# Kernel optimization log

Hardware: AMD Instinct MI355X
Metric: run time of the kernel (lower is better)

## Reference

```python
import jax, jax.numpy as jnp
import numpy as np

NUM_HEADS = 8
LN_EPS = 1e-5


def layer_norm_chw(x, w, b):
    # LayerNorm over (C, H, W) jointly, elementwise affine of shape (C, H, W)
    mu = jnp.mean(x, axis=(1, 2, 3), keepdims=True)
    var = jnp.mean(jnp.square(x - mu), axis=(1, 2, 3), keepdims=True)
    return (x - mu) * jax.lax.rsqrt(var + LN_EPS) * w[None] + b[None]


def conv1x1(x, w, b):
    # 1x1 conv == per-pixel matmul. x: (B,C,H,W), w: (O,C), b: (O,)
    return jnp.einsum('bcxy,oc->boxy', x, w) + b[None, :, None, None]


def setup_inputs() -> dict:
    key = jax.random.key(0)
    ks = jax.random.split(key, 8)
    B, C, H, W = 16, 512, 64, 64
    Dq, Dv, Dh = 512, 512, 2048
    s = lambda fan_in: 1.0 / np.sqrt(fan_in)
    return {
        'x': jax.random.normal(ks[0], (B, C, H, W), jnp.float32),
        'ln1_w': jnp.ones((C, H, W), jnp.float32),
        'ln1_b': jnp.zeros((C, H, W), jnp.float32),
        'q_w': jax.random.normal(ks[1], (Dq, C), jnp.float32) * s(C),
        'q_b': jnp.zeros((Dq,), jnp.float32),
        'k_w': jax.random.normal(ks[2], (Dq, C), jnp.float32) * s(C),
        'k_b': jnp.zeros((Dq,), jnp.float32),
        'v_w': jax.random.normal(ks[3], (Dv, C), jnp.float32) * s(C),
        'v_b': jnp.zeros((Dv,), jnp.float32),
        'hu_w': jax.random.normal(ks[4], (C, Dv), jnp.float32) * s(Dv),
        'hu_b': jnp.zeros((C,), jnp.float32),
        'ln2_w': jnp.ones((C, H, W), jnp.float32),
        'ln2_b': jnp.zeros((C, H, W), jnp.float32),
        'ff1_w': jax.random.normal(ks[5], (Dh, C), jnp.float32) * s(C),
        'ff1_b': jnp.zeros((Dh,), jnp.float32),
        'ff2_w': jax.random.normal(ks[6], (C, Dh), jnp.float32) * s(Dh),
        'ff2_b': jnp.zeros((C,), jnp.float32),
    }


def reference(x, ln1_w, ln1_b, q_w, q_b, k_w, k_b, v_w, v_b,
              hu_w, hu_b, ln2_w, ln2_b, ff1_w, ff1_b, ff2_w, ff2_b):
    B, C, H, W = x.shape
    h = NUM_HEADS

    a = layer_norm_chw(x, ln1_w, ln1_b)
    Q = conv1x1(a, q_w, q_b)   # (B, Dq, H, W)
    K = conv1x1(a, k_w, k_b)   # (B, Dq, H, W)
    V = conv1x1(a, v_w, v_b)   # (B, Dv, H, W)

    Dq, Dv = Q.shape[1], V.shape[1]
    # softmax over channel dim for Q (per pixel, over all Dq channels)
    Q = jax.nn.softmax(Q, axis=1)
    # softmax over flattened spatial dim for K (per channel)
    K = jax.nn.softmax(K.reshape(B, Dq, H * W), axis=-1).reshape(B, Dq, H, W)

    # split heads: (B, h, d, H, W)
    Qh = Q.reshape(B, h, Dq // h, H, W)
    Kh = K.reshape(B, h, Dq // h, H, W)
    Vh = V.reshape(B, h, Dv // h, H, W)

    # linear attention: KV = sum_xy K ⊗ V, then per-pixel KV^T @ Q
    KV = jnp.einsum('bhkxy,bhvxy->bhkv', Kh, Vh)        # (B, h, dq, dv)
    attn = jnp.einsum('bhkv,bhkxy->bhvxy', KV, Qh)      # (B, h, dv, H, W)
    attn = attn.reshape(B, Dv, H, W)
    attn = conv1x1(attn, hu_w, hu_b)                    # (B, C, H, W)

    x = x + attn
    x = layer_norm_chw(x, ln2_w, ln2_b)
    ff = conv1x1(jax.nn.gelu(conv1x1(x, ff1_w, ff1_b), approximate=False), ff2_w, ff2_b)
    return x + ff
```

## Files before the change

kernel.cpp:

```cpp
#include <hip/hip_runtime.h>
#include <math.h>

#define BATCH 16
#define CCH   512
#define HWS   4096
#define CHW   (CCH*HWS)
#define DHFF  2048
#define NHEAD 8
#define HD    64
#define QKVLD 1536
#define LNEPS 1e-5f

typedef unsigned short u16;
typedef __bf16 bf16x8 __attribute__((ext_vector_type(8)));
typedef float f32x4 __attribute__((ext_vector_type(4)));

__device__ __forceinline__ float gelu_f(float x) {
    float y = 1.5957691216057308f * x * (1.0f + 0.044715f * x * x);
    return x / (1.0f + __expf(-y));
}
__device__ __forceinline__ u16 f2bf(float f) {
    union { float f; unsigned u; } c; c.f = f;
    unsigned r = c.u + 0x7FFFu + ((c.u >> 16) & 1u);
    return (u16)(r >> 16);
}
__device__ __forceinline__ float bf2f(u16 h) {
    union { unsigned u; float f; } c; c.u = ((unsigned)h) << 16; return c.f;
}
__device__ __forceinline__ void gld16(const u16* g, u16* l) {
    __builtin_amdgcn_global_load_lds((const __attribute__((address_space(1))) unsigned*)g,
                                     (__attribute__((address_space(3))) unsigned*)l, 16, 0, 0);
}

__global__ __launch_bounds__(256) void stats_k(const float* __restrict__ src,
                                               float* __restrict__ st) {
    int b = blockIdx.y;
    const float4* p = (const float4*)(src + (size_t)b * CHW + (size_t)blockIdx.x * (CHW / 64));
    float s = 0.f, ss = 0.f;
    for (int i = threadIdx.x; i < (CHW / 64 / 4); i += 256) {
        float4 v = p[i];
        s  += v.x + v.y + v.z + v.w;
        ss += v.x * v.x + v.y * v.y + v.z * v.z + v.w * v.w;
    }
    __shared__ float r1[256], r2[256];
    int t = threadIdx.x;
    r1[t] = s; r2[t] = ss; __syncthreads();
    for (int o = 128; o > 0; o >>= 1) {
        if (t < o) { r1[t] += r1[t + o]; r2[t] += r2[t + o]; }
        __syncthreads();
    }
    if (t == 0) { atomicAdd(&st[2 * b], r1[0]); atomicAdd(&st[2 * b + 1], r2[0]); }
}

__global__ __launch_bounds__(256) void cvt_k(const float* __restrict__ src,
                                             u16* __restrict__ dst, int n4) {
    int i = blockIdx.x * 256 + threadIdx.x;
    if (i >= n4) return;
    float4 v = ((const float4*)src)[i];
    uint2 o; u16* op = (u16*)&o;
    op[0] = f2bf(v.x); op[1] = f2bf(v.y); op[2] = f2bf(v.z); op[3] = f2bf(v.w);
    ((uint2*)dst)[i] = o;
}

__global__ __launch_bounds__(256) void tr_k(const float* __restrict__ src,
                                            float* __restrict__ dst) {
    int p0 = blockIdx.x * 32, c0 = blockIdx.y * 32;
    __shared__ float T[32][33];
    int tx = threadIdx.x & 31, ty = threadIdx.x >> 5;
#pragma unroll
    for (int i = 0; i < 4; ++i)
        T[ty + i * 8][tx] = src[(size_t)(c0 + ty + i * 8) * HWS + p0 + tx];
    __syncthreads();
#pragma unroll
    for (int i = 0; i < 4; ++i)
        dst[(size_t)(p0 + ty + i * 8) * CCH + c0 + tx] = T[tx][ty + i * 8];
}

__global__ __launch_bounds__(256) void ln1t_k(const float* __restrict__ x,
                                              const float* __restrict__ w,
                                              const float* __restrict__ bb,
                                              const float* __restrict__ st,
                                              u16* __restrict__ a, int cb) {
    int p0 = blockIdx.x * 32, c0 = blockIdx.y * 32, bl = blockIdx.z;
    int b = cb + bl;
    float mean = st[2 * b] * (1.0f / CHW);
    float var  = st[2 * b + 1] * (1.0f / CHW) - mean * mean;
    float rstd = rsqrtf(var + LNEPS);
    __shared__ float T[32][33];
    int tx = threadIdx.x & 31, ty = threadIdx.x >> 5;
    const float* xb = x + (size_t)b * CHW;
#pragma unroll
    for (int i = 0; i < 4; ++i) {
        size_t o = (size_t)(c0 + ty + i * 8) * HWS + p0 + tx;
        T[ty + i * 8][tx] = (xb[o] - mean) * rstd * w[o] + bb[o];
    }
    __syncthreads();
    u16* ab = a + (size_t)bl * CHW;
#pragma unroll
    for (int i = 0; i < 4; ++i)
        ab[(size_t)(p0 + ty + i * 8) * CCH + c0 + tx] = f2bf(T[tx][ty + i * 8]);
}

template<int ACT, int OBF>
__global__ __launch_bounds__(256) void gemm_tn(const u16* __restrict__ A,
                                               const u16* __restrict__ B,
                                               const float* __restrict__ bias,
                                               void* __restrict__ Out,
                                               int K, int ldo, int nt) {
    __shared__ u16 As[128 * 32];
    __shared__ u16 Bs[128 * 32];
    const int tid = threadIdx.x;
    const int cpx = gridDim.x >> 3;
    const int wg = (blockIdx.x & 7) * cpx + (blockIdx.x >> 3);
    const int m0 = (wg / nt) * 128;
    const int n0 = (wg % nt) * 128;
    const int lane = tid & 63;
    const int w = tid >> 6;
    const int wm = (w & 1) * 64, wn = (w >> 1) * 64;
    const int ls = lane & 15, lq = lane >> 4;

    f32x4 acc[4][4];
#pragma unroll
    for (int i = 0; i < 4; ++i)
#pragma unroll
        for (int j = 0; j < 4; ++j) acc[i][j] = (f32x4){0.f, 0.f, 0.f, 0.f};

    const int srow = w * 16 + (lane >> 2);
    const int scol = (lane & 3) * 8;
    const u16* gA0 = A + (size_t)(m0 + srow) * K + scol;
    const u16* gA1 = gA0 + (size_t)64 * K;
    const u16* gB0 = B + (size_t)(n0 + srow) * K + scol;
    const u16* gB1 = gB0 + (size_t)64 * K;
    u16* lA0 = As + w * 512;
    u16* lA1 = As + 2048 + w * 512;
    u16* lB0 = Bs + w * 512;
    u16* lB1 = Bs + 2048 + w * 512;

    for (int kt = 0; kt < K; kt += 32) {
        __syncthreads();
        gld16(gA0 + kt, lA0);
        gld16(gA1 + kt, lA1);
        gld16(gB0 + kt, lB0);
        gld16(gB1 + kt, lB1);
        __syncthreads();
        bf16x8 af[4], bfv[4];
#pragma unroll
        for (int i = 0; i < 4; ++i)
            af[i] = *(bf16x8*)&As[(wm + i * 16 + ls) * 32 + lq * 8];
#pragma unroll
        for (int j = 0; j < 4; ++j)
            bfv[j] = *(bf16x8*)&Bs[(wn + j * 16 + ls) * 32 + lq * 8];
#pragma unroll
        for (int i = 0; i < 4; ++i)
#pragma unroll
            for (int j = 0; j < 4; ++j)
                acc[i][j] = __builtin_amdgcn_mfma_f32_16x16x32_bf16(bfv[j], af[i], acc[i][j], 0, 0, 0);
    }

#pragma unroll
    for (int j = 0; j < 4; ++j) {
        int nb = n0 + wn + j * 16 + lq * 4;
        float4 bv = *(const float4*)&bias[nb];
#pragma unroll
        for (int i = 0; i < 4; ++i) {
            int m = m0 + wm + i * 16 + ls;
            float v0 = acc[i][j][0] + bv.x;
            float v1 = acc[i][j][1] + bv.y;
            float v2 = acc[i][j][2] + bv.z;
            float v3 = acc[i][j][3] + bv.w;
            if (ACT) { v0 = gelu_f(v0); v1 = gelu_f(v1); v2 = gelu_f(v2); v3 = gelu_f(v3); }
            size_t idx = (size_t)m * ldo + nb;
            if (OBF) {
                uint2 o; u16* op = (u16*)&o;
                op[0] = f2bf(v0); op[1] = f2bf(v1); op[2] = f2bf(v2); op[3] = f2bf(v3);
                *(uint2*)((u16*)Out + idx) = o;
            } else {
                *(float4*)((float*)Out + idx) = (float4){v0, v1, v2, v3};
            }
        }
    }
}

__global__ __launch_bounds__(256) void softmax_row_k(u16* __restrict__ QKV) {
    int m = blockIdx.x * 4 + (threadIdx.x >> 6);
    int lane = threadIdx.x & 63;
    u16* row = QKV + (size_t)m * QKVLD + lane * 8;
    uint4 raw = *(uint4*)row;
    u16* pr = (u16*)&raw;
    float v[8];
#pragma unroll
    for (int i = 0; i < 8; ++i) v[i] = bf2f(pr[i]);
    float mx = v[0];
#pragma unroll
    for (int i = 1; i < 8; ++i) mx = fmaxf(mx, v[i]);
    for (int o = 32; o > 0; o >>= 1) mx = fmaxf(mx, __shfl_xor(mx, o, 64));
    float s = 0.f;
#pragma unroll
    for (int i = 0; i < 8; ++i) { v[i] = __expf(v[i] - mx); s += v[i]; }
    for (int o = 32; o > 0; o >>= 1) s += __shfl_xor(s, o, 64);
    float inv = 1.0f / s;
#pragma unroll
    for (int i = 0; i < 8; ++i) pr[i] = f2bf(v[i] * inv);
    *(uint4*)row = raw;
}

__global__ __launch_bounds__(256) void kcolstat_k(const u16* __restrict__ QKV,
                                                  float* __restrict__ kpart) {
    int pc = blockIdx.x, bl = blockIdx.y;
    int cg = threadIdx.x & 63;
    int ps = threadIdx.x >> 6;
    const u16* base = QKV + (size_t)bl * HWS * QKVLD + CCH + cg * 8;
    int p0 = pc * 256 + ps * 64;
    float m[8];
#pragma unroll
    for (int i = 0; i < 8; ++i) m[i] = -1e30f;
    for (int p = p0; p < p0 + 64; ++p) {
        uint4 r = *(const uint4*)(base + (size_t)p * QKVLD);
        u16* rp = (u16*)&r;
#pragma unroll
        for (int i = 0; i < 8; ++i) m[i] = fmaxf(m[i], bf2f(rp[i]));
    }
    __shared__ float red[4][512];
#pragma unroll
    for (int i = 0; i < 8; ++i) red[ps][cg * 8 + i] = m[i];
    __syncthreads();
#pragma unroll
    for (int i = 0; i < 8; ++i)
        m[i] = fmaxf(fmaxf(red[0][cg * 8 + i], red[1][cg * 8 + i]),
                     fmaxf(red[2][cg * 8 + i], red[3][cg * 8 + i]));
    __syncthreads();
    float s[8];
#pragma unroll
    for (int i = 0; i < 8; ++i) s[i] = 0.f;
    for (int p = p0; p < p0 + 64; ++p) {
        uint4 r = *(const uint4*)(base + (size_t)p * QKVLD);
        u16* rp = (u16*)&r;
#pragma unroll
        for (int i = 0; i < 8; ++i) s[i] += __expf(bf2f(rp[i]) - m[i]);
    }
#pragma unroll
    for (int i = 0; i < 8; ++i) red[ps][cg * 8 + i] = s[i];
    __syncthreads();
    if (ps == 0) {
        float* outp = kpart + (((size_t)bl * 16 + pc) * 512 + cg * 8) * 2;
#pragma unroll
        for (int i = 0; i < 8; ++i) {
            float sv = red[0][cg * 8 + i] + red[1][cg * 8 + i] +
                       red[2][cg * 8 + i] + red[3][cg * 8 + i];
            outp[2 * i] = m[i]; outp[2 * i + 1] = sv;
        }
    }
}

__global__ __launch_bounds__(256) void kcolmerge_k(const float* __restrict__ kpart,
                                                   float* __restrict__ kstat) {
    int bl = blockIdx.x;
#pragma unroll
    for (int j = 0; j < 2; ++j) {
        int col = threadIdx.x * 2 + j;
        float m = -1e30f;
        for (int pc = 0; pc < 16; ++pc)
            m = fmaxf(m, kpart[(((size_t)bl * 16 + pc) * 512 + col) * 2]);
        float s = 0.f;
        for (int pc = 0; pc < 16; ++pc) {
            const float* p = kpart + (((size_t)bl * 16 + pc) * 512 + col) * 2;
            s += p[1] * __expf(p[0] - m);
        }
        kstat[((size_t)bl * 512 + col) * 2]     = m;
        kstat[((size_t)bl * 512 + col) * 2 + 1] = 1.0f / s;
    }
}

__global__ __launch_bounds__(256) void kv_k2(const u16* __restrict__ QKV,
                                             const float* __restrict__ kstat,
                                             float* __restrict__ KV) {
    int pc = blockIdx.x, h = blockIdx.y, bl = blockIdx.z;
    const u16* kbase = QKV + (size_t)bl * HWS * QKVLD + CCH + h * HD;
    const u16* vbase = kbase + CCH;
    float* kvb = KV + ((size_t)bl * NHEAD + h) * (HD * HD);
    __shared__ float Ks[64][65], Vs[64][65];
    __shared__ float Ms[64], Is[64];
    int tid = threadIdx.x;
    if (tid < 64) {
        const float* sp = kstat + ((size_t)bl * 512 + h * HD + tid) * 2;
        Ms[tid] = sp[0]; Is[tid] = sp[1];
    }
    int tk = tid >> 4, tv = tid & 15;
    float acc[4][4];
#pragma unroll
    for (int i = 0; i < 4; ++i)
#pragma unroll
        for (int j = 0; j < 4; ++j) acc[i][j] = 0.f;

    for (int s = 0; s < 4; ++s) {
        int pbase = pc * 256 + s * 64;
        __syncthreads();
#pragma unroll
        for (int j = 0; j < 2; ++j) {
            int li = tid + j * 256;
            int pl = li >> 3, c8 = (li & 7) * 8;
            uint4 kr = *(const uint4*)(kbase + (size_t)(pbase + pl) * QKVLD + c8);
            uint4 vr = *(const uint4*)(vbase + (size_t)(pbase + pl) * QKVLD + c8);
            u16* kp = (u16*)&kr; u16* vp = (u16*)&vr;
#pragma unroll
            for (int t = 0; t < 8; ++t) {
                Ks[pl][c8 + t] = __expf(bf2f(kp[t]) - Ms[c8 + t]) * Is[c8 + t];
                Vs[pl][c8 + t] = bf2f(vp[t]);
            }
        }
        __syncthreads();
#pragma unroll 4
        for (int p = 0; p < 64; ++p) {
            float ka[4], va[4];
#pragma unroll
            for (int i = 0; i < 4; ++i) { ka[i] = Ks[p][tk * 4 + i]; va[i] = Vs[p][tv * 4 + i]; }
#pragma unroll
            for (int i = 0; i < 4; ++i)
#pragma unroll
                for (int j = 0; j < 4; ++j) acc[i][j] += ka[i] * va[j];
        }
    }
#pragma unroll
    for (int i = 0; i < 4; ++i)
#pragma unroll
        for (int j = 0; j < 4; ++j)
            atomicAdd(&kvb[(size_t)(tk * 4 + i) * HD + tv * 4 + j], acc[i][j]);
}

__global__ __launch_bounds__(256) void attn_k2(const u16* __restrict__ QKV,
                                               const float* __restrict__ KV,
                                               u16* __restrict__ attnRaw) {
    int pt = blockIdx.x, h = blockIdx.y, bl = blockIdx.z;
    const u16* qbase = QKV + (size_t)bl * HWS * QKVLD + h * HD;
    const float* kvb = KV + ((size_t)bl * NHEAD + h) * (HD * HD);
    __shared__ float KVs[64][68], Qs[64][68];
    int tid = threadIdx.x;
#pragma unroll
    for (int j = 0; j < 4; ++j) {
        int li = tid + j * 256;
        int k = li >> 4, c4 = (li & 15) * 4;
        *(float4*)&KVs[k][c4] = *(const float4*)(kvb + (size_t)k * HD + c4);
    }
#pragma unroll
    for (int j = 0; j < 2; ++j) {
        int li = tid + j * 256;
        int pl = li >> 3, c8 = (li & 7) * 8;
        uint4 qr = *(const uint4*)(qbase + (size_t)(pt * 64 + pl) * QKVLD + c8);
        u16* qp = (u16*)&qr;
#pragma unroll
        for (int t = 0; t < 8; ++t) Qs[pl][c8 + t] = bf2f(qp[t]);
    }
    __syncthreads();
    int tp = tid >> 4, tv = tid & 15;
    float acc[4][4];
#pragma unroll
    for (int i = 0; i < 4; ++i)
#pragma unroll
        for (int j = 0; j < 4; ++j) acc[i][j] = 0.f;
#pragma unroll 4
    for (int k = 0; k < 64; ++k) {
        float qa[4], kv4[4];
#pragma unroll
        for (int i = 0; i < 4; ++i) { qa[i] = Qs[tp * 4 + i][k]; kv4[i] = KVs[k][tv * 4 + i]; }
#pragma unroll
        for (int i = 0; i < 4; ++i)
#pragma unroll
            for (int j = 0; j < 4; ++j) acc[i][j] += qa[i] * kv4[j];
    }
#pragma unroll
    for (int i = 0; i < 4; ++i) {
        uint2 wv; u16* wp = (u16*)&wv;
#pragma unroll
        for (int j = 0; j < 4; ++j) wp[j] = f2bf(acc[i][j]);
        *(uint2*)(attnRaw + (size_t)(bl * HWS + pt * 64 + tp * 4 + i) * CCH + h * HD + tv * 4) = wv;
    }
}

__global__ __launch_bounds__(256) void resid_t_k(const float* __restrict__ x,
                                                 const float* __restrict__ ao,
                                                 float* __restrict__ r,
                                                 float* __restrict__ pstat, int cb) {
    int p0 = blockIdx.x * 32, c0 = blockIdx.y * 32, bl = blockIdx.z;
    int b = cb + bl;
    __shared__ float T[32][33];
    __shared__ float r1[256], r2[256];
    int tx = threadIdx.x & 31, ty = threadIdx.x >> 5;
    const float* xb = x + (size_t)b * CHW;
#pragma unroll
    for (int i = 0; i < 4; ++i)
        T[ty + i * 8][tx] = xb[(size_t)(c0 + ty + i * 8) * HWS + p0 + tx];
    __syncthreads();
    float s = 0.f, ss = 0.f;
#pragma unroll
    for (int i = 0; i < 4; ++i) {
        size_t o = (size_t)bl * CHW + (size_t)(p0 + ty + i * 8) * CCH + c0 + tx;
        float v = T[tx][ty + i * 8] + ao[o];
        r[o] = v; s += v; ss += v * v;
    }
    int t = threadIdx.x;
    r1[t] = s; r2[t] = ss; __syncthreads();
    for (int o = 128; o > 0; o >>= 1) {
        if (t < o) { r1[t] += r1[t + o]; r2[t] += r2[t + o]; }
        __syncthreads();
    }
    if (t == 0) {
        float* pp = pstat + ((size_t)b * 2048 + (size_t)blockIdx.x * 16 + blockIdx.y) * 2;
        pp[0] = r1[0]; pp[1] = r2[0];
    }
}

__global__ __launch_bounds__(256) void red2_k(const float* __restrict__ pstat,
                                              float* __restrict__ st, int cb) {
    int b = cb + blockIdx.x;
    const float* p = pstat + (size_t)b * 4096;
    float s = 0.f, ss = 0.f;
    for (int i = threadIdx.x; i < 2048; i += 256) {
        s += p[2 * i]; ss += p[2 * i + 1];
    }
    __shared__ float r1[256], r2[256];
    int t = threadIdx.x;
    r1[t] = s; r2[t] = ss; __syncthreads();
    for (int o = 128; o > 0; o >>= 1) {
        if (t < o) { r1[t] += r1[t + o]; r2[t] += r2[t + o]; }
        __syncthreads();
    }
    if (t == 0) { st[32 + 2 * b] = r1[0]; st[32 + 2 * b + 1] = r2[0]; }
}

__global__ __launch_bounds__(256) void ln2a_k(const float* __restrict__ r,
                                              const float* __restrict__ w2t,
                                              const float* __restrict__ b2t,
                                              const float* __restrict__ st,
                                              u16* __restrict__ x2, int cb) {
    size_t i4 = (size_t)blockIdx.x * 256 + threadIdx.x;
    int bl = (int)(i4 / (CHW / 4));
    int b = cb + bl;
    size_t off4 = i4 % (CHW / 4);
    float mean = st[32 + 2 * b] * (1.0f / CHW);
    float var  = st[32 + 2 * b + 1] * (1.0f / CHW) - mean * mean;
    float rstd = rsqrtf(var + LNEPS);
    float4 v  = ((const float4*)(r + (size_t)bl * CHW))[off4];
    float4 wv = ((const float4*)w2t)[off4];
    float4 bv = ((const float4*)b2t)[off4];
    uint2 o; u16* op = (u16*)&o;
    op[0] = f2bf((v.x - mean) * rstd * wv.x + bv.x);
    op[1] = f2bf((v.y - mean) * rstd * wv.y + bv.y);
    op[2] = f2bf((v.z - mean) * rstd * wv.z + bv.z);
    op[3] = f2bf((v.w - mean) * rstd * wv.w + bv.w);
    ((uint2*)(x2 + (size_t)bl * CHW))[off4] = o;
}

__global__ __launch_bounds__(256) void final_t_k(const u16* __restrict__ x2,
                                                 const float* __restrict__ ffo,
                                                 float* __restrict__ out, int cb) {
    int c0 = blockIdx.x * 32, p0 = blockIdx.y * 32, bl = blockIdx.z;
    int b = cb + bl;
    __shared__ float T[32][33];
    int tx = threadIdx.x & 31, ty = threadIdx.x >> 5;
#pragma unroll
    for (int i = 0; i < 4; ++i) {
        size_t o = (size_t)bl * CHW + (size_t)(p0 + ty + i * 8) * CCH + c0 + tx;
        T[ty + i * 8][tx] = ffo[o] + bf2f(x2[o]);
    }
    __syncthreads();
    float* ob = out + (size_t)b * CHW;
#pragma unroll
    for (int i = 0; i < 4; ++i)
        ob[(size_t)(c0 + ty + i * 8) * HWS + p0 + tx] = T[tx][ty + i * 8];
}

extern "C" void kernel_launch(void* const* d_in, const int* in_sizes, int n_in,
                              void* d_out, int out_size, void* d_ws, size_t ws_size,
                              hipStream_t stream) {
    const float* x    = (const float*)d_in[0];
    const float* ln1w = (const float*)d_in[1];
    const float* ln1b = (const float*)d_in[2];
    const float* qw   = (const float*)d_in[3];
    const float* qb   = (const float*)d_in[4];
    const float* kw   = (const float*)d_in[5];
    const float* kb   = (const float*)d_in[6];
    const float* vw   = (const float*)d_in[7];
    const float* vb   = (const float*)d_in[8];
    const float* huw  = (const float*)d_in[9];
    const float* hub  = (const float*)d_in[10];
    const float* ln2w = (const float*)d_in[11];
    const float* ln2b = (const float*)d_in[12];
    const float* f1w  = (const float*)d_in[13];
    const float* f1b  = (const float*)d_in[14];
    const float* f2w  = (const float*)d_in[15];
    const float* f2b  = (const float*)d_in[16];
    float* out = (float*)d_out;
    float* ws = (float*)d_ws;

    float* stats = ws;
    float* qkvb  = ws + 64;
    u16*   wqkv  = (u16*)(ws + 1600);
    u16*   whu   = (u16*)(ws + 394816);
    u16*   wf1   = (u16*)(ws + 525888);
    u16*   wf2   = (u16*)(ws + 1050176);
    float* w2t   = ws + 1574464;
    float* b2t   = ws + 3671616;
    float* pstat = ws + 5768768;
    float* kpart = ws + 5834304;
    float* kstat = ws + 6096448;
    float* kvbuf = ws + 6112832;

    int G = 16;
    while (G > 1 && (6112832ull + (size_t)G * 7372800ull) * 4ull > ws_size) G >>= 1;
    const int nch = BATCH / G;
    const size_t U = (size_t)G * CHW;

    float* R       = kvbuf + (size_t)G * 32768;
    u16*   a_bf    = (u16*)R;
    u16*   QKVb    = (u16*)(R + U / 2);
    float* attnOut = R + U / 2;
    float* rbuf    = R + 3 * U / 2;
    u16*   x2bf    = (u16*)R;
    u16*   Hbuf    = (u16*)(R + U / 2);
    float* ffOut   = R + 5 * U / 2;

    hipMemsetAsync(stats, 0, 64 * sizeof(float), stream);

    cvt_k<<<dim3(256), 256, 0, stream>>>(qw, wqkv, 65536);
    cvt_k<<<dim3(256), 256, 0, stream>>>(kw, wqkv + 262144, 65536);
    cvt_k<<<dim3(256), 256, 0, stream>>>(vw, wqkv + 524288, 65536);
    cvt_k<<<dim3(256), 256, 0, stream>>>(huw, whu, 65536);
    cvt_k<<<dim3(1024), 256, 0, stream>>>(f1w, wf1, 262144);
    cvt_k<<<dim3(1024), 256, 0, stream>>>(f2w, wf2, 262144);
    tr_k<<<dim3(128, 16), 256, 0, stream>>>(ln2w, w2t);
    tr_k<<<dim3(128, 16), 256, 0, stream>>>(ln2b, b2t);
    hipMemcpyAsync(qkvb,        qb, 512 * sizeof(float), hipMemcpyDeviceToDevice, stream);
    hipMemcpyAsync(qkvb + 512,  kb, 512 * sizeof(float), hipMemcpyDeviceToDevice, stream);
    hipMemcpyAsync(qkvb + 1024, vb, 512 * sizeof(float), hipMemcpyDeviceToDevice, stream);

    stats_k<<<dim3(64, BATCH), 256, 0, stream>>>(x, stats);

    for (int g = 0; g < nch; ++g) {
        const int cb = g * G;
        const int mt = G * 32;
        ln1t_k<<<dim3(128, 16, G), 256, 0, stream>>>(x, ln1w, ln1b, stats, a_bf, cb);
        gemm_tn<0, 1><<<dim3(mt * 12), 256, 0, stream>>>(a_bf, wqkv, qkvb, QKVb, CCH, QKVLD, 12);
        softmax_row_k<<<dim3(G * 1024), 256, 0, stream>>>(QKVb);
        kcolstat_k<<<dim3(16, G), 256, 0, stream>>>(QKVb, kpart);
        kcolmerge_k<<<dim3(G), 256, 0, stream>>>(kpart, kstat);
        hipMemsetAsync(kvbuf, 0, (size_t)G * 32768 * sizeof(float), stream);
        kv_k2<<<dim3(16, NHEAD, G), 256, 0, stream>>>(QKVb, kstat, kvbuf);
        attn_k2<<<dim3(64, NHEAD, G), 256, 0, stream>>>(QKVb, kvbuf, a_bf);
        gemm_tn<0, 0><<<dim3(mt * 4), 256, 0, stream>>>(a_bf, whu, hub, attnOut, CCH, CCH, 4);
        resid_t_k<<<dim3(128, 16, G), 256, 0, stream>>>(x, attnOut, rbuf, pstat, cb);
        red2_k<<<dim3(G), 256, 0, stream>>>(pstat, stats, cb);
        ln2a_k<<<dim3(G * 2048), 256, 0, stream>>>(rbuf, w2t, b2t, stats, x2bf, cb);
        gemm_tn<1, 1><<<dim3(mt * 16), 256, 0, stream>>>(x2bf, wf1, f1b, Hbuf, CCH, DHFF, 16);
        gemm_tn<0, 0><<<dim3(mt * 4), 256, 0, stream>>>(Hbuf, wf2, f2b, ffOut, DHFF, CCH, 4);
        final_t_k<<<dim3(16, 128, G), 256, 0, stream>>>(x2bf, ffOut, out, cb);
    }
}
```

Before: 1.571 ms.

## Double-buffer LDS tiles in GEMM to overlap global loads with MFMA

Gives the bf16 GEMM kernel two LDS buffers for the A and B tiles. The next K-slice is prefetched with direct-to-LDS loads while MFMAs run on the current slice, and the per-iteration barrier count drops from two to one. The aim is to hide global memory latency behind compute, at the cost of doubling LDS use per block, which may lower occupancy.

```diff
diff --git a/kernel.cpp b/kernel.cpp
--- a/kernel.cpp
+++ b/kernel.cpp
@@ -107,8 +107,8 @@
                                                const float* __restrict__ bias,
                                                void* __restrict__ Out,
                                                int K, int ldo, int nt) {
-    __shared__ u16 As[128 * 32];
-    __shared__ u16 Bs[128 * 32];
+    __shared__ u16 As[2][128 * 32];
+    __shared__ u16 Bs[2][128 * 32];
     const int tid = threadIdx.x;
     const int cpx = gridDim.x >> 3;
     const int wg = (blockIdx.x & 7) * cpx + (blockIdx.x >> 3);
@@ -131,30 +131,39 @@
     const u16* gA1 = gA0 + (size_t)64 * K;
     const u16* gB0 = B + (size_t)(n0 + srow) * K + scol;
     const u16* gB1 = gB0 + (size_t)64 * K;
-    u16* lA0 = As + w * 512;
-    u16* lA1 = As + 2048 + w * 512;
-    u16* lB0 = Bs + w * 512;
-    u16* lB1 = Bs + 2048 + w * 512;
-
+    const int lo = w * 512;
+
+    gld16(gA0, &As[0][lo]);
+    gld16(gA1, &As[0][2048 + lo]);
+    gld16(gB0, &Bs[0][lo]);
+    gld16(gB1, &Bs[0][2048 + lo]);
+    __syncthreads();
+
+    int cur = 0;
     for (int kt = 0; kt < K; kt += 32) {
-        __syncthreads();
-        gld16(gA0 + kt, lA0);
-        gld16(gA1 + kt, lA1);
-        gld16(gB0 + kt, lB0);
-        gld16(gB1 + kt, lB1);
-        __syncthreads();
+        if (kt + 32 < K) {
+            int nx = cur ^ 1;
+            gld16(gA0 + kt + 32, &As[nx][lo]);
+            gld16(gA1 + kt + 32, &As[nx][2048 + lo]);
+            gld16(gB0 + kt + 32, &Bs[nx][lo]);
+            gld16(gB1 + kt + 32, &Bs[nx][2048 + lo]);
+        }
         bf16x8 af[4], bfv[4];
 #pragma unroll
         for (int i = 0; i < 4; ++i)
-            af[i] = *(bf16x8*)&As[(wm + i * 16 + ls) * 32 + lq * 8];
+            af[i] = *(bf16x8*)&As[cur][(wm + i * 16 + ls) * 32 + lq * 8];
 #pragma unroll
         for (int j = 0; j < 4; ++j)
-            bfv[j] = *(bf16x8*)&Bs[(wn + j * 16 + ls) * 32 + lq * 8];
+            bfv[j] = *(bf16x8*)&Bs[cur][(wn + j * 16 + ls) * 32 + lq * 8];
 #pragma unroll
         for (int i = 0; i < 4; ++i)
 #pragma unroll
             for (int j = 0; j < 4; ++j)
                 acc[i][j] = __builtin_amdgcn_mfma_f32_16x16x32_bf16(bfv[j], af[i], acc[i][j], 0, 0, 0);
+        if (kt + 32 < K) {
+            __syncthreads();
+            cur ^= 1;
+        }
     }
 
 #pragma unroll
```

New measurement: 1.731 ms. 10.2% more time.
